# Optimization experiments

Measured on AMD Instinct MI355X. Metric: run time of the kernel, lower is better.

The kernel has to match this reference:

```python
import jax, jax.numpy as jnp
import numpy as np

FP8_MAX = 448.0  # finfo(float8_e4m3fn).max
EPS = 1e-12
BLK = 128        # weight_block_size = (128, 128); activation group_size = 128


def setup_inputs() -> dict:
    key = jax.random.key(0)
    k1, k2, k3, k4 = jax.random.split(key, 4)
    B, S, H, O = 4, 4096, 2048, 2048
    x = jax.random.normal(k1, (B, S, H), dtype=jnp.float32)
    # fp8 weight: generate, round to e4m3fn grid, store as f32 (values exactly fp8-representable)
    w_raw = jax.random.normal(k2, (O, H), dtype=jnp.float32) * 0.02
    weight = w_raw.astype(jnp.float8_e4m3fn).astype(jnp.float32)
    # per-(128x128)-block weight scales
    weight_scale = jax.random.uniform(k3, (O // BLK, H // BLK), dtype=jnp.float32,
                                      minval=0.001, maxval=0.01)
    bias = jax.random.normal(k4, (O,), dtype=jnp.float32) * 0.01
    return {"x": x, "weight": weight, "weight_scale": weight_scale, "bias": bias}


def reference(x, weight, weight_scale, bias):
    B, S, H = x.shape
    O = weight.shape[0]
    J = H // BLK  # number of activation groups / weight column-blocks
    # per-token-group fp8 quantization (group_size = BLK)
    xg = x.reshape(-1, J, BLK)                                      # [M, J, BLK]
    max_abs = jnp.clip(jnp.max(jnp.abs(xg), axis=-1, keepdims=True), EPS)
    scales = FP8_MAX / max_abs                                      # [M, J, 1]
    xq = jnp.clip(xg * scales, -FP8_MAX, FP8_MAX)
    xq = xq.astype(jnp.float8_e4m3fn).astype(jnp.float32)           # fp8 round-trip
    inv_scale = 1.0 / scales                                        # stored input_scale
    # block-scaled matmul == dequantize both operands then single GEMM
    x_dq = (xq * inv_scale).reshape(-1, H)                          # [M, H]
    w_scale_full = jnp.repeat(jnp.repeat(weight_scale, BLK, axis=0), BLK, axis=1)  # [O, H]
    w_dq = weight * w_scale_full                                    # [O, H]
    y = x_dq @ w_dq.T + bias                                        # [M, O]
    return y.reshape(B, S, O)
```

## Files before the change

kernel.cpp:

```cpp
#include <hip/hip_runtime.h>
#include <cstdint>

#define FP8MAX 448.0f

typedef float f32x4 __attribute__((ext_vector_type(4)));
typedef int   i32x4 __attribute__((ext_vector_type(4)));
typedef int   i32x8 __attribute__((ext_vector_type(8)));

union frag8 { i32x8 v8; i32x4 v4[2]; };

__device__ __forceinline__ void gload_lds16(const void* g, void* l) {
  __builtin_amdgcn_global_load_lds(
      (const __attribute__((address_space(1))) unsigned int*)g,
      (__attribute__((address_space(3))) unsigned int*)l,
      16, 0, 0);
}

__global__ __launch_bounds__(256) void quant_x(const float* __restrict__ x,
                                               uint8_t* __restrict__ xq,
                                               float* __restrict__ sa) {
  const int m = blockIdx.x;
  const int t = threadIdx.x;
  const float* xr = x + (size_t)m * 2048;
  float4 v0 = ((const float4*)xr)[t * 2];
  float4 v1 = ((const float4*)xr)[t * 2 + 1];
  float amax = fmaxf(fmaxf(fmaxf(fabsf(v0.x), fabsf(v0.y)), fmaxf(fabsf(v0.z), fabsf(v0.w))),
                     fmaxf(fmaxf(fabsf(v1.x), fabsf(v1.y)), fmaxf(fabsf(v1.z), fabsf(v1.w))));
  #pragma unroll
  for (int off = 1; off < 16; off <<= 1)
    amax = fmaxf(amax, __shfl_xor(amax, off));
  amax = fmaxf(amax, 1e-12f);
  float s   = FP8MAX / amax;
  float inv = 1.0f / s;
  if ((t & 15) == 0) sa[(size_t)m * 16 + (t >> 4)] = inv;
  float q[8] = {v0.x * s, v0.y * s, v0.z * s, v0.w * s,
                v1.x * s, v1.y * s, v1.z * s, v1.w * s};
  #pragma unroll
  for (int i = 0; i < 8; ++i) q[i] = fminf(fmaxf(q[i], -FP8MAX), FP8MAX);
  union { unsigned long long u; unsigned int w[2]; } pk;
  pk.w[0] = __builtin_amdgcn_cvt_pk_fp8_f32(q[0], q[1], 0, false);
  pk.w[0] = __builtin_amdgcn_cvt_pk_fp8_f32(q[2], q[3], pk.w[0], true);
  pk.w[1] = __builtin_amdgcn_cvt_pk_fp8_f32(q[4], q[5], 0, false);
  pk.w[1] = __builtin_amdgcn_cvt_pk_fp8_f32(q[6], q[7], pk.w[1], true);
  ((unsigned long long*)(xq + (size_t)m * 2048))[t] = pk.u;
}

__global__ __launch_bounds__(256) void conv_w(const float* __restrict__ w,
                                              uint8_t* __restrict__ w8, int n8) {
  int i = blockIdx.x * 256 + threadIdx.x;
  if (i >= n8) return;
  float4 v0 = ((const float4*)w)[i * 2];
  float4 v1 = ((const float4*)w)[i * 2 + 1];
  union { unsigned long long u; unsigned int x[2]; } pk;
  pk.x[0] = __builtin_amdgcn_cvt_pk_fp8_f32(v0.x, v0.y, 0, false);
  pk.x[0] = __builtin_amdgcn_cvt_pk_fp8_f32(v0.z, v0.w, pk.x[0], true);
  pk.x[1] = __builtin_amdgcn_cvt_pk_fp8_f32(v1.x, v1.y, 0, false);
  pk.x[1] = __builtin_amdgcn_cvt_pk_fp8_f32(v1.z, v1.w, pk.x[1], true);
  ((unsigned long long*)w8)[i] = pk.u;
}

#define SAL_STRIDE 264

__global__ __launch_bounds__(512, 2) void gemm_fp8(
    const uint8_t* __restrict__ A, const uint8_t* __restrict__ Bw,
    const float* __restrict__ sa, const float* __restrict__ sb,
    const float* __restrict__ bias, float* __restrict__ out,
    int M, int N, int K) {
  const int J = K >> 7;
  const int nbn = N >> 8;
  int bid = blockIdx.x;
  int nwg = gridDim.x;
  if ((nwg & 7) == 0) {
    int cpx = nwg >> 3;
    bid = (bid & 7) * cpx + (bid >> 3);
  }
  const int bn = bid % nbn;
  const int bm = bid / nbn;
  const int t = threadIdx.x;
  const int lane = t & 63;
  const int w = t >> 6;
  const int wr = w >> 2;
  const int wc = w & 3;
  const int r16 = lane & 15;
  const int kg = lane >> 4;

  __shared__ __align__(16) uint8_t lA[2][256 * 128];
  __shared__ __align__(16) uint8_t lB[2][256 * 128];
  __shared__ __align__(16) float sal[16 * SAL_STRIDE];

  const uint8_t* gA = A + (size_t)bm * 256 * K;
  const uint8_t* gB = Bw + (size_t)bn * 256 * K;

  for (int i = t; i < 256 * 16; i += 512) {
    int row = i >> 4, j = i & 15;
    sal[j * SAL_STRIDE + row] = sa[((size_t)bm * 256 + row) * 16 + j];
  }

  const int rl = t >> 3;
  const int sg = t & 7;

  #define STAGE(larr, gbase, h_, kt_) do {                                   \
    _Pragma("unroll")                                                        \
    for (int it_ = 0; it_ < 2; ++it_) {                                      \
      int r_ = it_ * 64 + rl;                                                \
      int grow_ = (h_) * 128 + r_;                                           \
      gload_lds16(gbase + (size_t)grow_ * K + (size_t)(kt_) * 128 +          \
                      ((sg ^ (r_ & 7)) << 4),                                \
                  &larr[grow_ * 128 + sg * 16]);                             \
    } } while (0)

  __syncthreads();

  STAGE(lA[0], gA, 0, 0);
  STAGE(lB[0], gB, 0, 0);
  STAGE(lB[0], gB, 1, 0);
  STAGE(lA[0], gA, 1, 0);

  f32x4 tot[8][4] = {};
  const f32x4 fz = {0.f, 0.f, 0.f, 0.f};
  frag8 av[4], bv[2][2];
  f32x4 scq[4];

  #define BARSEQ(NN) do {                                                    \
    asm volatile("s_waitcnt vmcnt(" #NN ")" ::: "memory");                   \
    __builtin_amdgcn_s_barrier();                                            \
    asm volatile("" ::: "memory"); } while (0)

  #define READ_A(mg_, cur_) do { _Pragma("unroll")                           \
    for (int i_ = 0; i_ < 4; ++i_) {                                         \
      int row_ = (mg_) * 128 + wr * 64 + i_ * 16 + r16;                      \
      const uint8_t* bp_ = &lA[cur_][row_ * 128];                            \
      int sw_ = (row_ & 7) << 4;                                             \
      av[i_].v4[0] = *(const i32x4*)(bp_ + ((kg * 32) ^ sw_));               \
      av[i_].v4[1] = *(const i32x4*)(bp_ + ((kg * 32 + 16) ^ sw_));          \
    } } while (0)

  #define READ_B(ng_, cur_) do { _Pragma("unroll")                           \
    for (int j_ = 0; j_ < 2; ++j_) {                                         \
      int row_ = (ng_) * 128 + wc * 32 + j_ * 16 + r16;                      \
      const uint8_t* bp_ = &lB[cur_][row_ * 128];                            \
      int sw_ = (row_ & 7) << 4;                                             \
      bv[ng_][j_].v4[0] = *(const i32x4*)(bp_ + ((kg * 32) ^ sw_));          \
      bv[ng_][j_].v4[1] = *(const i32x4*)(bp_ + ((kg * 32 + 16) ^ sw_));     \
    } } while (0)

  #define CALC_SC(mg_, kt_, sbj_) do { _Pragma("unroll")                     \
    for (int i_ = 0; i_ < 4; ++i_) {                                         \
      scq[i_] = (*(const f32x4*)&sal[(kt_) * SAL_STRIDE + (mg_) * 128 +      \
                                     wr * 64 + i_ * 16 + kg * 4]) * (sbj_);  \
    } } while (0)

  #define MFMA8(mg_, ng_) do {                                               \
    __builtin_amdgcn_s_setprio(1);                                           \
    _Pragma("unroll")                                                        \
    for (int i_ = 0; i_ < 4; ++i_) { _Pragma("unroll")                       \
      for (int j_ = 0; j_ < 2; ++j_) {                                       \
        f32x4 p_ = __builtin_amdgcn_mfma_scale_f32_16x16x128_f8f6f4(         \
            av[i_].v8, bv[ng_][j_].v8, fz, 0, 0, 0, 0x7f7f7f7f, 0,           \
            0x7f7f7f7f);                                                     \
        tot[(mg_) * 4 + i_][(ng_) * 2 + j_] += p_ * scq[i_];                 \
      } }                                                                    \
    __builtin_amdgcn_s_setprio(0); } while (0)

  const int KT = K >> 7;
  for (int kt = 0; kt < KT - 1; ++kt) {
    const int cur = kt & 1, nxt = cur ^ 1;
    const float sb0 = sb[(bn * 2 + 0) * J + kt];
    const float sb1 = sb[(bn * 2 + 1) * J + kt];
    BARSEQ(4);
    READ_A(0, cur); READ_B(0, cur);
    STAGE(lA[nxt], gA, 0, kt + 1);
    CALC_SC(0, kt, sb0);
    MFMA8(0, 0);
    BARSEQ(4);
    READ_B(1, cur);
    STAGE(lB[nxt], gB, 0, kt + 1);
    CALC_SC(0, kt, sb1);
    MFMA8(0, 1);
    BARSEQ(4);
    READ_A(1, cur);
    STAGE(lB[nxt], gB, 1, kt + 1);
    CALC_SC(1, kt, sb0);
    MFMA8(1, 0);
    STAGE(lA[nxt], gA, 1, kt + 1);
    CALC_SC(1, kt, sb1);
    MFMA8(1, 1);
  }
  {
    const int kt = KT - 1, cur = kt & 1;
    const float sb0 = sb[(bn * 2 + 0) * J + kt];
    const float sb1 = sb[(bn * 2 + 1) * J + kt];
    BARSEQ(4);
    READ_A(0, cur); READ_B(0, cur);
    CALC_SC(0, kt, sb0); MFMA8(0, 0);
    BARSEQ(2);
    READ_B(1, cur);
    CALC_SC(0, kt, sb1); MFMA8(0, 1);
    BARSEQ(0);
    READ_A(1, cur);
    CALC_SC(1, kt, sb0); MFMA8(1, 0);
    CALC_SC(1, kt, sb1); MFMA8(1, 1);
  }

  #pragma unroll
  for (int ng = 0; ng < 2; ++ng) {
    float bb[2];
    #pragma unroll
    for (int j = 0; j < 2; ++j)
      bb[j] = bias[bn * 256 + ng * 128 + wc * 32 + j * 16 + r16];
    #pragma unroll
    for (int mg = 0; mg < 2; ++mg) {
      #pragma unroll
      for (int i = 0; i < 4; ++i) {
        int row0 = bm * 256 + mg * 128 + wr * 64 + i * 16 + kg * 4;
        #pragma unroll
        for (int r = 0; r < 4; ++r) {
          float* orow = out + (size_t)(row0 + r) * N + bn * 256 + ng * 128 + wc * 32;
          #pragma unroll
          for (int j = 0; j < 2; ++j)
            orow[j * 16 + r16] = tot[mg * 4 + i][ng * 2 + j][r] + bb[j];
        }
      }
    }
  }
}

extern "C" void kernel_launch(void* const* d_in, const int* in_sizes, int n_in,
                              void* d_out, int out_size, void* d_ws, size_t ws_size,
                              hipStream_t stream) {
  const float* x    = (const float*)d_in[0];
  const float* wt   = (const float*)d_in[1];
  const float* wsc  = (const float*)d_in[2];
  const float* bias = (const float*)d_in[3];
  float* out = (float*)d_out;

  const int O = in_sizes[3];
  const int H = in_sizes[1] / O;
  const int M = in_sizes[0] / H;

  uint8_t* xq = (uint8_t*)d_ws;
  uint8_t* w8 = xq + (size_t)M * H;
  float*   sa = (float*)(w8 + (size_t)O * H);

  quant_x<<<M, 256, 0, stream>>>(x, xq, sa);
  int n8 = O * H / 8;
  conv_w<<<(n8 + 255) / 256, 256, 0, stream>>>(wt, w8, n8);
  int grid = (M / 256) * (O / 256);
  gemm_fp8<<<grid, 512, 0, stream>>>(xq, w8, sa, wsc, bias, out, M, O, H);
}
```

Before: 158.3 us.

## Deepen GEMM K-loop prefetch with 2x-unrolled half-tile staging and split barriers

Restructures the FP8 block-scaled GEMM main loop so it processes two K-tiles per iteration and prefetches half-tiles up to two K-steps ahead. The prologue preloads an extra half of the next buffer. Each MFMA phase is now wrapped in explicit barriers, with an LDS-read wait (lgkmcnt) and a sched_barrier before it, and the vmcnt waits are loosened. The aim is to hide global-to-LDS latency behind more compute and to keep LDS reads from overlapping MFMA issue. In exchange it adds barriers per K-step, and the wrapped index issues redundant loads of early tiles at the tail, which are waited on at the end.

```diff
diff --git a/kernel.cpp b/kernel.cpp
--- a/kernel.cpp
+++ b/kernel.cpp
@@ -99,46 +99,53 @@
   const int rl = t >> 3;
   const int sg = t & 7;
 
-  #define STAGE(larr, gbase, h_, kt_) do {                                   \
+  #define STAGE(ldst, gbase, h_, kt_) do {                                   \
     _Pragma("unroll")                                                        \
     for (int it_ = 0; it_ < 2; ++it_) {                                      \
       int r_ = it_ * 64 + rl;                                                \
-      int grow_ = (h_) * 128 + r_;                                           \
-      gload_lds16(gbase + (size_t)grow_ * K + (size_t)(kt_) * 128 +          \
+      int gr_ = (h_) * 128 + r_;                                             \
+      gload_lds16(gbase + (size_t)gr_ * K + ((kt_) << 7) +                   \
                       ((sg ^ (r_ & 7)) << 4),                                \
-                  &larr[grow_ * 128 + sg * 16]);                             \
+                  (ldst) + gr_ * 128 + sg * 16);                             \
     } } while (0)
 
   __syncthreads();
 
   STAGE(lA[0], gA, 0, 0);
   STAGE(lB[0], gB, 0, 0);
+  STAGE(lA[0], gA, 1, 0);
   STAGE(lB[0], gB, 1, 0);
-  STAGE(lA[0], gA, 1, 0);
+  STAGE(lA[1], gA, 0, 1);
+  STAGE(lB[1], gB, 0, 1);
 
   f32x4 tot[8][4] = {};
   const f32x4 fz = {0.f, 0.f, 0.f, 0.f};
   frag8 av[4], bv[2][2];
   f32x4 scq[4];
 
-  #define BARSEQ(NN) do {                                                    \
-    asm volatile("s_waitcnt vmcnt(" #NN ")" ::: "memory");                   \
-    __builtin_amdgcn_s_barrier();                                            \
-    asm volatile("" ::: "memory"); } while (0)
-
-  #define READ_A(mg_, cur_) do { _Pragma("unroll")                           \
+  #define BAR1_VM8  do { asm volatile("s_waitcnt vmcnt(8)" ::: "memory");    \
+                         __builtin_amdgcn_s_barrier();                       \
+                         asm volatile("" ::: "memory"); } while (0)
+  #define BAR1      do { __builtin_amdgcn_s_barrier();                       \
+                         asm volatile("" ::: "memory"); } while (0)
+  #define MID       do { asm volatile("s_waitcnt lgkmcnt(0)" ::: "memory");  \
+                         __builtin_amdgcn_sched_barrier(0); } while (0)
+  #define BAR2      do { __builtin_amdgcn_s_barrier();                       \
+                         asm volatile("" ::: "memory"); } while (0)
+
+  #define READ_A(mg_, buf_) do { _Pragma("unroll")                           \
     for (int i_ = 0; i_ < 4; ++i_) {                                         \
       int row_ = (mg_) * 128 + wr * 64 + i_ * 16 + r16;                      \
-      const uint8_t* bp_ = &lA[cur_][row_ * 128];                            \
+      const uint8_t* bp_ = &lA[buf_][row_ * 128];                            \
       int sw_ = (row_ & 7) << 4;                                             \
       av[i_].v4[0] = *(const i32x4*)(bp_ + ((kg * 32) ^ sw_));               \
       av[i_].v4[1] = *(const i32x4*)(bp_ + ((kg * 32 + 16) ^ sw_));          \
     } } while (0)
 
-  #define READ_B(ng_, cur_) do { _Pragma("unroll")                           \
+  #define READ_B(ng_, buf_) do { _Pragma("unroll")                           \
     for (int j_ = 0; j_ < 2; ++j_) {                                         \
       int row_ = (ng_) * 128 + wc * 32 + j_ * 16 + r16;                      \
-      const uint8_t* bp_ = &lB[cur_][row_ * 128];                            \
+      const uint8_t* bp_ = &lB[buf_][row_ * 128];                            \
       int sw_ = (row_ & 7) << 4;                                             \
       bv[ng_][j_].v4[0] = *(const i32x4*)(bp_ + ((kg * 32) ^ sw_));          \
       bv[ng_][j_].v4[1] = *(const i32x4*)(bp_ + ((kg * 32 + 16) ^ sw_));     \
@@ -163,44 +170,47 @@
     __builtin_amdgcn_s_setprio(0); } while (0)
 
   const int KT = K >> 7;
-  for (int kt = 0; kt < KT - 1; ++kt) {
-    const int cur = kt & 1, nxt = cur ^ 1;
-    const float sb0 = sb[(bn * 2 + 0) * J + kt];
-    const float sb1 = sb[(bn * 2 + 1) * J + kt];
-    BARSEQ(4);
-    READ_A(0, cur); READ_B(0, cur);
-    STAGE(lA[nxt], gA, 0, kt + 1);
-    CALC_SC(0, kt, sb0);
-    MFMA8(0, 0);
-    BARSEQ(4);
-    READ_B(1, cur);
-    STAGE(lB[nxt], gB, 0, kt + 1);
-    CALC_SC(0, kt, sb1);
-    MFMA8(0, 1);
-    BARSEQ(4);
-    READ_A(1, cur);
-    STAGE(lB[nxt], gB, 1, kt + 1);
-    CALC_SC(1, kt, sb0);
-    MFMA8(1, 0);
-    STAGE(lA[nxt], gA, 1, kt + 1);
+  const int NI = KT >> 1;
+  for (int i = 0; i < NI; ++i) {
+    const int kt = 2 * i;
+    const int kt2 = (kt + 2 < KT) ? kt + 2 : kt + 2 - KT;
+    const int kt3 = (kt + 3 < KT) ? kt + 3 : kt + 3 - KT;
+    const float sb0  = sb[(bn * 2 + 0) * J + kt];
+    const float sb1  = sb[(bn * 2 + 1) * J + kt];
+    const float sb0n = sb[(bn * 2 + 0) * J + kt + 1];
+    const float sb1n = sb[(bn * 2 + 1) * J + kt + 1];
+    BAR1_VM8;
+    READ_A(0, 0); READ_B(0, 0); CALC_SC(0, kt, sb0);
+    STAGE(lA[1], gA, 1, kt + 1); STAGE(lB[1], gB, 1, kt + 1);
+    MID; MFMA8(0, 0); BAR2;
+    BAR1_VM8;
+    READ_B(1, 0); CALC_SC(0, kt, sb1);
+    MID; MFMA8(0, 1); BAR2;
+    BAR1;
+    READ_A(1, 0); CALC_SC(1, kt, sb0);
+    STAGE(lA[0], gA, 0, kt2);
+    MID; MFMA8(1, 0); BAR2;
+    BAR1;
     CALC_SC(1, kt, sb1);
-    MFMA8(1, 1);
-  }
-  {
-    const int kt = KT - 1, cur = kt & 1;
-    const float sb0 = sb[(bn * 2 + 0) * J + kt];
-    const float sb1 = sb[(bn * 2 + 1) * J + kt];
-    BARSEQ(4);
-    READ_A(0, cur); READ_B(0, cur);
-    CALC_SC(0, kt, sb0); MFMA8(0, 0);
-    BARSEQ(2);
-    READ_B(1, cur);
-    CALC_SC(0, kt, sb1); MFMA8(0, 1);
-    BARSEQ(0);
-    READ_A(1, cur);
-    CALC_SC(1, kt, sb0); MFMA8(1, 0);
-    CALC_SC(1, kt, sb1); MFMA8(1, 1);
-  }
+    STAGE(lB[0], gB, 0, kt2);
+    MID; MFMA8(1, 1); BAR2;
+    BAR1_VM8;
+    READ_A(0, 1); READ_B(0, 1); CALC_SC(0, kt + 1, sb0n);
+    STAGE(lA[0], gA, 1, kt2); STAGE(lB[0], gB, 1, kt2);
+    MID; MFMA8(0, 0); BAR2;
+    BAR1_VM8;
+    READ_B(1, 1); CALC_SC(0, kt + 1, sb1n);
+    MID; MFMA8(0, 1); BAR2;
+    BAR1;
+    READ_A(1, 1); CALC_SC(1, kt + 1, sb0n);
+    STAGE(lA[1], gA, 0, kt3);
+    MID; MFMA8(1, 0); BAR2;
+    BAR1;
+    CALC_SC(1, kt + 1, sb1n);
+    STAGE(lB[1], gB, 0, kt3);
+    MID; MFMA8(1, 1); BAR2;
+  }
+  asm volatile("s_waitcnt vmcnt(0)" ::: "memory");
 
   #pragma unroll
   for (int ng = 0; ng < 2; ++ng) {
```

Result: no change. 156.0 us (-1.5%).
